# Performance work log

Hardware: AMD Instinct MI355X
Metric: run time of the kernel (lower is better)

Reference implementation:

```python
import jax, jax.numpy as jnp
import numpy as np

B, T, N, F = 32, 24, 1024, 2   # batch, seq_len, num_adj, num_feature
HID = 32                       # opt['hidden_dim']
U = HID // 2                   # rnn_units = 16
TF = 31                        # opt['time_feature']


def setup_inputs():
    key = jax.random.key(0)
    ks = jax.random.split(key, 40)
    def nrm(k, shape):
        return jax.random.normal(k, shape, dtype=jnp.float32) * 0.05
    inp = {}
    inp['recent_data'] = nrm(ks[0], (B, T, N, F))
    inp['trend_data'] = nrm(ks[1], (B, T, F))
    # normalized adjacency-like matrix (non-negative, row mass ~1)
    inp['sub_graph'] = jax.random.uniform(ks[2], (B, N, N), dtype=jnp.float32) * (2.0 / N)
    inp['time_feature'] = nrm(ks[3], (B, TF))
    i = 4
    for layer, insz in ((1, F + U), (2, U + U)):
        for g in 'ruc':
            inp[f'gru{layer}_{g}W'] = nrm(ks[i], (U, insz)); i += 1
            inp[f'gru{layer}_{g}b'] = jnp.zeros((U,), jnp.float32)
    for l, insz in ((0, F), (1, HID)):
        inp[f'lstm_Wih{l}'] = nrm(ks[i], (4 * HID, insz)); i += 1
        inp[f'lstm_Whh{l}'] = nrm(ks[i], (4 * HID, HID)); i += 1
        inp[f'lstm_bih{l}'] = jnp.zeros((4 * HID,), jnp.float32)
        inp[f'lstm_bhh{l}'] = jnp.zeros((4 * HID,), jnp.float32)
    inp['ff_W'] = nrm(ks[i], (HID, TF)); i += 1
    inp['ff_b'] = jnp.zeros((HID,), jnp.float32)
    inp['gcn_W'] = nrm(ks[i], (F, int(HID * 2.5))); i += 1
    inp['gcn_b'] = jnp.zeros((F,), jnp.float32)
    return inp


def _gcn(x, A, W, b, act):
    # x: (B,N,in), A: (B,N,N) -> act(fc(A @ x)): (B,N,out)
    return act(jnp.einsum('bij,bjf->bif', A, x) @ W.T + b)


def _gru_cell(x, h, A, rW, rb, uW, ub, cW, cb):
    xh = jnp.concatenate([x, h], axis=-1)
    r = _gcn(xh, A, rW, rb, jax.nn.sigmoid)
    u = _gcn(xh, A, uW, ub, jax.nn.sigmoid)
    c = _gcn(jnp.concatenate([x, r * h], axis=-1), A, cW, cb, jnp.tanh)
    return u * h + (1.0 - u) * c


def _lstm_layer(xs, Wih, Whh, bih, bhh):
    # xs: (T, B, in) -> hidden sequence (T, B, H); PyTorch gate order i,f,g,o
    H = Whh.shape[1]
    z = jnp.zeros((xs.shape[1], H), xs.dtype)
    def step(carry, x_t):
        h, c = carry
        g = x_t @ Wih.T + h @ Whh.T + bih + bhh
        i, f, gg, o = jnp.split(g, 4, axis=-1)
        c = jax.nn.sigmoid(f) * c + jax.nn.sigmoid(i) * jnp.tanh(gg)
        h = jax.nn.sigmoid(o) * jnp.tanh(c)
        return (h, c), h
    _, hs = jax.lax.scan(step, (z, z), xs)
    return hs


def _forward(recent_data, trend_data, sub_graph, time_feature,
             gru1_rW, gru1_rb, gru1_uW, gru1_ub, gru1_cW, gru1_cb,
             gru2_rW, gru2_rb, gru2_uW, gru2_ub, gru2_cW, gru2_cb,
             lstm_Wih0, lstm_Whh0, lstm_bih0, lstm_bhh0,
             lstm_Wih1, lstm_Whh1, lstm_bih1, lstm_bhh1,
             ff_W, ff_b, gcn_W, gcn_b):
    b, t, n, _ = recent_data.shape
    u = gru1_rW.shape[0]
    h0 = jnp.zeros((b, n, u), recent_data.dtype)
    # 2-layer GCGRU encoder over time (only final output/state is used)
    def step(carry, x_t):
        h1, h2 = carry
        h1 = _gru_cell(x_t, h1, sub_graph, gru1_rW, gru1_rb, gru1_uW, gru1_ub, gru1_cW, gru1_cb)
        h2 = _gru_cell(h1, h2, sub_graph, gru2_rW, gru2_rb, gru2_uW, gru2_ub, gru2_cW, gru2_cb)
        return (h1, h2), None
    (h1, h2), _ = jax.lax.scan(step, (h0, h0), jnp.swapaxes(recent_data, 0, 1))
    recent = h2  # (B, N, U)
    # 2-layer LSTM on trend_data; take last timestep hidden
    xs = jnp.swapaxes(trend_data, 0, 1)  # (T, B, F)
    hs = _lstm_layer(xs, lstm_Wih0, lstm_Whh0, lstm_bih0, lstm_bhh0)
    hs = _lstm_layer(hs, lstm_Wih1, lstm_Whh1, lstm_bih1, lstm_bhh1)
    trend = jnp.broadcast_to(hs[-1][:, None, :], (b, n, hs.shape[-1]))
    feat = jax.nn.relu(time_feature @ ff_W.T + ff_b)
    feat = jnp.broadcast_to(feat[:, None, :], (b, n, feat.shape[-1]))
    combined = jnp.concatenate([recent, trend, feat], axis=-1)  # (B, N, 2.5*HID)
    return _gcn(combined, sub_graph, gcn_W, gcn_b, jnp.tanh)  # (B, N, F)


def reference(recent_data, trend_data, sub_graph, time_feature,
              gru1_rW, gru1_rb, gru1_uW, gru1_ub, gru1_cW, gru1_cb,
              gru2_rW, gru2_rb, gru2_uW, gru2_ub, gru2_cW, gru2_cb,
              lstm_Wih0, lstm_Whh0, lstm_bih0, lstm_bhh0,
              lstm_Wih1, lstm_Whh1, lstm_bih1, lstm_bhh1,
              ff_W, ff_b, gcn_W, gcn_b):
    return _forward(recent_data, trend_data, sub_graph, time_feature,
                    gru1_rW, gru1_rb, gru1_uW, gru1_ub, gru1_cW, gru1_cb,
                    gru2_rW, gru2_rb, gru2_uW, gru2_ub, gru2_cW, gru2_cb,
                    lstm_Wih0, lstm_Whh0, lstm_bih0, lstm_bhh0,
                    lstm_Wih1, lstm_Whh1, lstm_bih1, lstm_bhh1,
                    ff_W, ff_b, gcn_W, gcn_b)
```

## Files before the change

kernel.cpp:

```cpp
#include <hip/hip_runtime.h>
#include <cmath>
#include <stdint.h>

#define BB 32
#define TT 24
#define NN 1024
#define FF 2
#define UU 16
#define HH 32
#define TFN 31
#define NWG 256

typedef __attribute__((ext_vector_type(8))) short bf16x8;
typedef __attribute__((ext_vector_type(4))) float f32x4;
typedef unsigned short u16;
typedef unsigned int   u32;
typedef __attribute__((ext_vector_type(4))) u32 u32x4;

__device__ __align__(16) u16 g_Y[2][BB][32*NN];
__device__ float g_c2[BB*FF];
__device__ __align__(256) u32 g_bar[BB][64];
__device__ u32 g_xcdmask[BB];

__device__ __forceinline__ float sigmf(float x){ return 1.f/(1.f+expf(-x)); }
__device__ __forceinline__ u16 f2bf(float f){
  u32 u = __float_as_uint(f);
  return (u16)((u + 0x7fffu + ((u>>16)&1u)) >> 16);
}
__device__ __forceinline__ void ywr(u16* Yb, int j, int n, float s, bool modeA){
  u16* p = (u16*)((char*)Yb + (j<<11) + (((n<<1)) ^ ((j&7)<<4)));
  u16 v = f2bf(s);
  if (modeA) *p = v;
  else __hip_atomic_store(p, v, __ATOMIC_RELAXED, __HIP_MEMORY_SCOPE_AGENT);
}

__device__ __forceinline__ void bbar(u32* cnt, u32 target){
  __syncthreads();
  if (threadIdx.x == 0){
    __hip_atomic_fetch_add(cnt, 1u, __ATOMIC_RELAXED, __HIP_MEMORY_SCOPE_AGENT);
    while (__hip_atomic_load(cnt, __ATOMIC_RELAXED, __HIP_MEMORY_SCOPE_AGENT) < target)
      __builtin_amdgcn_s_sleep(1);
  }
  __syncthreads();
}

template<int W>
__device__ __forceinline__ void stageY(const u16* __restrict__ Yb, u16* Ys,
                                       int tid, bool modeA){
  u32x4 r[W/4];
  if (modeA){
#pragma unroll
    for (int q=0;q<W/4;q++){
      const char* src = (const char*)Yb + q*8192 + tid*16;
      asm volatile("global_load_dwordx4 %0, %1, off sc0"
                   : "=v"(r[q]) : "v"(src));
    }
  } else {
#pragma unroll
    for (int q=0;q<W/4;q++){
      const char* src = (const char*)Yb + q*8192 + tid*16;
      asm volatile("global_load_dwordx4 %0, %1, off sc0 sc1"
                   : "=v"(r[q]) : "v"(src));
    }
  }
  asm volatile("s_waitcnt vmcnt(0)" ::: "memory");
  __builtin_amdgcn_sched_barrier(0);
#pragma unroll
  for (int q=0;q<W/4;q++)
    *(u32x4*)((char*)Ys + q*8192 + tid*16) = r[q];
}

__device__ __forceinline__ void mm32(const bf16x8 (&areg)[32], const u16* Ys,
                                     int base0, int cflip, f32x4& a0, f32x4& a1){
#pragma unroll
  for (int c=0;c<32;c++){
    int off = base0 + ((c ^ cflip) << 6);
    bf16x8 b0 = *(const bf16x8*)((const char*)Ys + off);
    bf16x8 b1 = *(const bf16x8*)((const char*)Ys + off + 32768);
    a0 = __builtin_amdgcn_mfma_f32_16x16x32_bf16(areg[c], b0, a0, 0, 0, 0);
    a1 = __builtin_amdgcn_mfma_f32_16x16x32_bf16(areg[c], b1, a1, 0, 0, 0);
  }
}
__device__ __forceinline__ void mm16(const bf16x8 (&areg)[32], const u16* Ys,
                                     int base0, int cflip, f32x4& a0){
#pragma unroll
  for (int c=0;c<32;c++){
    int off = base0 + ((c ^ cflip) << 6);
    bf16x8 b0 = *(const bf16x8*)((const char*)Ys + off);
    a0 = __builtin_amdgcn_mfma_f32_16x16x32_bf16(areg[c], b0, a0, 0, 0, 0);
  }
}

__global__ __launch_bounds__(128)
void k_lstm(const float* __restrict__ trend, const float* __restrict__ tfeat,
            const float* __restrict__ Wih0, const float* __restrict__ Whh0,
            const float* __restrict__ bih0, const float* __restrict__ bhh0,
            const float* __restrict__ Wih1, const float* __restrict__ Whh1,
            const float* __restrict__ bih1, const float* __restrict__ bhh1,
            const float* __restrict__ ffW, const float* __restrict__ ffb,
            const float* __restrict__ gcnW) {
  __shared__ float h[HH], c[HH], g[4*HH], hs0[TT][HH], tr[HH], fe[HH];
  int b = blockIdx.x, tid = threadIdx.x;
  if (tid == 0){
    __hip_atomic_store(&g_bar[b][0], 0u, __ATOMIC_RELAXED, __HIP_MEMORY_SCOPE_AGENT);
    __hip_atomic_store(&g_xcdmask[b], 0u, __ATOMIC_RELAXED, __HIP_MEMORY_SCOPE_AGENT);
  }
  if (tid < HH) { h[tid]=0.f; c[tid]=0.f; }
  __syncthreads();
  for (int t=0;t<TT;t++) {
    float x0 = trend[(b*TT+t)*FF+0], x1 = trend[(b*TT+t)*FF+1];
    float gv = bih0[tid] + bhh0[tid] + x0*Wih0[tid*FF+0] + x1*Wih0[tid*FF+1];
#pragma unroll
    for (int k=0;k<HH;k++) gv += h[k]*Whh0[tid*HH+k];
    g[tid] = gv;
    __syncthreads();
    if (tid < HH) {
      float ii = sigmf(g[tid]), ff = sigmf(g[HH+tid]);
      float gg = tanhf(g[2*HH+tid]), oo = sigmf(g[3*HH+tid]);
      float cn = ff*c[tid] + ii*gg;
      c[tid] = cn;
      float hn = oo*tanhf(cn);
      h[tid] = hn;
      hs0[t][tid] = hn;
    }
    __syncthreads();
  }
  if (tid < HH) { h[tid]=0.f; c[tid]=0.f; }
  __syncthreads();
  for (int t=0;t<TT;t++) {
    float gv = bih1[tid] + bhh1[tid];
#pragma unroll
    for (int k=0;k<HH;k++) gv += hs0[t][k]*Wih1[tid*HH+k];
#pragma unroll
    for (int k=0;k<HH;k++) gv += h[k]*Whh1[tid*HH+k];
    g[tid] = gv;
    __syncthreads();
    if (tid < HH) {
      float ii = sigmf(g[tid]), ff = sigmf(g[HH+tid]);
      float gg = tanhf(g[2*HH+tid]), oo = sigmf(g[3*HH+tid]);
      float cn = ff*c[tid] + ii*gg;
      c[tid] = cn;
      h[tid] = oo*tanhf(cn);
    }
    __syncthreads();
  }
  if (tid < HH) {
    tr[tid] = h[tid];
    float fv = ffb[tid];
#pragma unroll
    for (int j=0;j<TFN;j++) fv += tfeat[b*TFN+j]*ffW[tid*TFN+j];
    fe[tid] = fmaxf(fv, 0.f);
  }
  __syncthreads();
  if (tid < FF) {
    float s = 0.f;
#pragma unroll
    for (int j=0;j<HH;j++) s += tr[j]*gcnW[tid*80+16+j];
#pragma unroll
    for (int j=0;j<HH;j++) s += fe[j]*gcnW[tid*80+48+j];
    g_c2[b*FF+tid] = s;
  }
}

struct KP {
  const float *recent, *A;
  const float *g1rW,*g1rb,*g1uW,*g1ub,*g1cW,*g1cb;
  const float *g2rW,*g2rb,*g2uW,*g2ub,*g2cW,*g2cb;
  const float *gcnW,*gcnb;
  float *out;
};

__global__ __launch_bounds__(512, 2)
void k_main(KP p){
  __shared__ __align__(16) u16 Ys[32*NN];
  __shared__ float Ps [128][33];
  __shared__ float h1s[128][17];
  __shared__ float h2s[128][17];
  __shared__ float us_[128][17];
  __shared__ float rhs[128][17];

  const int wg = blockIdx.x;
  const int b = (wg & 7)*4 + (wg >> 6);
  const int i0 = ((wg >> 3) & 7) << 7;
  const int tid = threadIdx.x;
  const int v = tid >> 6, lane = tid & 63, m = lane & 15, quad = lane >> 4;
  const int rloc = v << 4;
  const int row = tid >> 2, jj = tid & 3;
  const int n = i0 + row;
  const int base0 = m*2048 + ((quad ^ (m & 3)) << 4);
  const int cflip = (m >> 2) & 1;
  u32* bar = &g_bar[b][0];

  if (tid == 0){
    u32 xcc;
    asm volatile("s_getreg_b32 %0, hwreg(HW_REG_XCC_ID)" : "=s"(xcc));
    __hip_atomic_fetch_or(&g_xcdmask[b], 1u << (xcc & 31),
                          __ATOMIC_RELAXED, __HIP_MEMORY_SCOPE_AGENT);
  }

  bf16x8 areg[32];
  {
    const float* Ab = p.A + ((size_t)(b*NN + i0 + rloc + m))*NN + quad*8;
#pragma unroll
    for (int c=0;c<32;c++){
      float4 f0 = *(const float4*)(Ab + c*32);
      float4 f1 = *(const float4*)(Ab + c*32 + 4);
      bf16x8 tv;
      tv[0]=(short)f2bf(f0.x); tv[1]=(short)f2bf(f0.y);
      tv[2]=(short)f2bf(f0.z); tv[3]=(short)f2bf(f0.w);
      tv[4]=(short)f2bf(f1.x); tv[5]=(short)f2bf(f1.y);
      tv[6]=(short)f2bf(f1.z); tv[7]=(short)f2bf(f1.w);
      areg[c] = tv;
    }
  }

#pragma unroll
  for (int q=0;q<4;q++){ h1s[row][jj*4+q]=0.f; h2s[row][jj*4+q]=0.f; }

  {
    const float* xr = p.recent + (((size_t)b*TT)*NN + n)*FF;
    float x0 = xr[0], x1 = xr[1];
    u16* Yb = g_Y[0][b];
#pragma unroll
    for (int m2=0;m2<8;m2++){
      int j = jj*8 + m2;
      const float* W = (j<16) ? (p.g1rW + j*18) : (p.g1uW + (j-16)*18);
      ywr(Yb, j, n, x0*W[0] + x1*W[1], false);
    }
  }
  u32 gen = 0;
  bbar(bar, (++gen)*8);

  const u32 mk = __hip_atomic_load(&g_xcdmask[b], __ATOMIC_RELAXED,
                                   __HIP_MEMORY_SCOPE_AGENT);
  const bool modeA = (__popc(mk) == 1);

  int buf = 0;
  for (int t=0;t<TT;t++){
    stageY<32>(g_Y[buf][b], Ys, tid, modeA);
    __syncthreads();
    {
      f32x4 a0={0.f,0.f,0.f,0.f}, a1={0.f,0.f,0.f,0.f};
      mm32(areg, Ys, base0, cflip, a0, a1);
#pragma unroll
      for (int r=0;r<4;r++){
        Ps[rloc + quad*4 + r][m]    = a0[r];
        Ps[rloc + quad*4 + r][16+m] = a1[r];
      }
    }
    __syncthreads();
#pragma unroll
    for (int q=0;q<4;q++){
      int j = jj*4+q;
      float rv = sigmf(Ps[row][j]    + p.g1rb[j]);
      float uv = sigmf(Ps[row][16+j] + p.g1ub[j]);
      us_[row][j] = uv;
      rhs[row][j] = rv * h1s[row][j];
    }
    __syncthreads();
    {
      const float* xr = p.recent + (((size_t)b*TT + t)*NN + n)*FF;
      float x0 = xr[0], x1 = xr[1];
      u16* Yb = g_Y[buf^1][b];
#pragma unroll
      for (int q=0;q<4;q++){
        int j = jj*4+q;
        const float* W = p.g1cW + j*18;
        float s = fmaf(x0, W[0], x1*W[1]);
#pragma unroll
        for (int f=0;f<16;f++) s = fmaf(rhs[row][f], W[2+f], s);
        ywr(Yb, j, n, s, modeA);
      }
    }
    bbar(bar, (++gen)*8); buf ^= 1;

    stageY<16>(g_Y[buf][b], Ys, tid, modeA);
    __syncthreads();
    {
      f32x4 a0={0.f,0.f,0.f,0.f};
      mm16(areg, Ys, base0, cflip, a0);
#pragma unroll
      for (int r=0;r<4;r++) Ps[rloc + quad*4 + r][m] = a0[r];
    }
    __syncthreads();
#pragma unroll
    for (int q=0;q<4;q++){
      int j = jj*4+q;
      float cv = tanhf(Ps[row][j] + p.g1cb[j]);
      float uv = us_[row][j];
      h1s[row][j] = uv*h1s[row][j] + (1.f-uv)*cv;
    }
    __syncthreads();
    {
      u16* Yb = g_Y[buf^1][b];
#pragma unroll
      for (int m2=0;m2<8;m2++){
        int j = jj*8 + m2;
        const float* W = (j<16) ? (p.g2rW + j*32) : (p.g2uW + (j-16)*32);
        float s = 0.f;
#pragma unroll
        for (int f=0;f<16;f++) s = fmaf(h1s[row][f], W[f],    s);
#pragma unroll
        for (int f=0;f<16;f++) s = fmaf(h2s[row][f], W[16+f], s);
        ywr(Yb, j, n, s, modeA);
      }
    }
    bbar(bar, (++gen)*8); buf ^= 1;

    stageY<32>(g_Y[buf][b], Ys, tid, modeA);
    __syncthreads();
    {
      f32x4 a0={0.f,0.f,0.f,0.f}, a1={0.f,0.f,0.f,0.f};
      mm32(areg, Ys, base0, cflip, a0, a1);
#pragma unroll
      for (int r=0;r<4;r++){
        Ps[rloc + quad*4 + r][m]    = a0[r];
        Ps[rloc + quad*4 + r][16+m] = a1[r];
      }
    }
    __syncthreads();
#pragma unroll
    for (int q=0;q<4;q++){
      int j = jj*4+q;
      float rv = sigmf(Ps[row][j]    + p.g2rb[j]);
      float uv = sigmf(Ps[row][16+j] + p.g2ub[j]);
      us_[row][j] = uv;
      rhs[row][j] = rv * h2s[row][j];
    }
    __syncthreads();
    {
      u16* Yb = g_Y[buf^1][b];
#pragma unroll
      for (int q=0;q<4;q++){
        int j = jj*4+q;
        const float* W = p.g2cW + j*32;
        float s = 0.f;
#pragma unroll
        for (int f=0;f<16;f++) s = fmaf(h1s[row][f], W[f],    s);
#pragma unroll
        for (int f=0;f<16;f++) s = fmaf(rhs[row][f], W[16+f], s);
        ywr(Yb, j, n, s, modeA);
      }
    }
    bbar(bar, (++gen)*8); buf ^= 1;

    stageY<16>(g_Y[buf][b], Ys, tid, modeA);
    __syncthreads();
    {
      f32x4 a0={0.f,0.f,0.f,0.f};
      mm16(areg, Ys, base0, cflip, a0);
#pragma unroll
      for (int r=0;r<4;r++) Ps[rloc + quad*4 + r][m] = a0[r];
    }
    __syncthreads();
#pragma unroll
    for (int q=0;q<4;q++){
      int j = jj*4+q;
      float cv = tanhf(Ps[row][j] + p.g2cb[j]);
      float uv = us_[row][j];
      h2s[row][j] = uv*h2s[row][j] + (1.f-uv)*cv;
    }
    __syncthreads();
    if (t < TT-1){
      const float* xr = p.recent + (((size_t)b*TT + t + 1)*NN + n)*FF;
      float x0 = xr[0], x1 = xr[1];
      u16* Yb = g_Y[buf^1][b];
#pragma unroll
      for (int m2=0;m2<8;m2++){
        int j = jj*8 + m2;
        const float* W = (j<16) ? (p.g1rW + j*18) : (p.g1uW + (j-16)*18);
        float s = fmaf(x0, W[0], x1*W[1]);
#pragma unroll
        for (int f=0;f<16;f++) s = fmaf(h1s[row][f], W[2+f], s);
        ywr(Yb, j, n, s, modeA);
      }
    } else {
      u16* Yb = g_Y[buf^1][b];
#pragma unroll
      for (int q=0;q<4;q++){
        int j = jj*4+q;
        float s = 0.f;
        if (j < FF){
          s = g_c2[b*FF + j];
#pragma unroll
          for (int f=0;f<16;f++) s = fmaf(h2s[row][f], p.gcnW[j*80+f], s);
        }
        ywr(Yb, j, n, s, modeA);
      }
    }
    bbar(bar, (++gen)*8); buf ^= 1;
  }

  stageY<16>(g_Y[buf][b], Ys, tid, modeA);
  __syncthreads();
  {
    f32x4 a0={0.f,0.f,0.f,0.f};
    mm16(areg, Ys, base0, cflip, a0);
    if (m < FF){
      float bb = p.gcnb[m];
#pragma unroll
      for (int r=0;r<4;r++){
        int nn = i0 + rloc + quad*4 + r;
        p.out[((size_t)b*NN + nn)*FF + m] = tanhf(a0[r] + bb);
      }
    }
  }
}

extern "C" void kernel_launch(void* const* d_in, const int* in_sizes, int n_in,
                              void* d_out, int out_size, void* d_ws, size_t ws_size,
                              hipStream_t stream) {
  (void)in_sizes; (void)n_in; (void)d_ws; (void)ws_size; (void)out_size;
  const float* recent = (const float*)d_in[0];
  const float* trend  = (const float*)d_in[1];
  const float* A      = (const float*)d_in[2];
  const float* tfeat  = (const float*)d_in[3];
  const float* g1rW = (const float*)d_in[4];  const float* g1rb = (const float*)d_in[5];
  const float* g1uW = (const float*)d_in[6];  const float* g1ub = (const float*)d_in[7];
  const float* g1cW = (const float*)d_in[8];  const float* g1cb = (const float*)d_in[9];
  const float* g2rW = (const float*)d_in[10]; const float* g2rb = (const float*)d_in[11];
  const float* g2uW = (const float*)d_in[12]; const float* g2ub = (const float*)d_in[13];
  const float* g2cW = (const float*)d_in[14]; const float* g2cb = (const float*)d_in[15];
  const float* Wih0 = (const float*)d_in[16]; const float* Whh0 = (const float*)d_in[17];
  const float* bih0 = (const float*)d_in[18]; const float* bhh0 = (const float*)d_in[19];
  const float* Wih1 = (const float*)d_in[20]; const float* Whh1 = (const float*)d_in[21];
  const float* bih1 = (const float*)d_in[22]; const float* bhh1 = (const float*)d_in[23];
  const float* ffW  = (const float*)d_in[24]; const float* ffb  = (const float*)d_in[25];
  const float* gcnW = (const float*)d_in[26]; const float* gcnb = (const float*)d_in[27];
  float* out = (float*)d_out;

  k_lstm<<<BB, 128, 0, stream>>>(trend, tfeat, Wih0, Whh0, bih0, bhh0,
                                 Wih1, Whh1, bih1, bhh1, ffW, ffb, gcnW);

  KP kp;
  kp.recent = recent; kp.A = A;
  kp.g1rW=g1rW; kp.g1rb=g1rb; kp.g1uW=g1uW; kp.g1ub=g1ub; kp.g1cW=g1cW; kp.g1cb=g1cb;
  kp.g2rW=g2rW; kp.g2rb=g2rb; kp.g2uW=g2uW; kp.g2ub=g2ub; kp.g2cW=g2cW; kp.g2cb=g2cb;
  kp.gcnW=gcnW; kp.gcnb=gcnb; kp.out=out;
  void* args[] = { (void*)&kp };
  hipLaunchCooperativeKernel((const void*)k_main, dim3(NWG), dim3(512), args, 0, stream);
}
```

Baseline: 1.605 ms.

## Hoist next-step layer-1 GRU input into layer-2 phase to drop a grid barrier

Replaces the two ping-pong Y buffers with dedicated per-stage regions (two alternating RU1 slots, C1, RU2, C2). This lets the next timestep's layer-1 r/u projections be written during the layer-2 r/u phase, removing one cross-workgroup barrier per timestep (4 instead of 5). The barrier spin also gets an iteration cap and a longer sleep after a few polls. The cap risks proceeding early under contention, and the longer sleep can add wake-up latency.

After: 1.638 ms. 1.02x slower.

```diff
diff --git a/kernel.cpp b/kernel.cpp
--- a/kernel.cpp
+++ b/kernel.cpp
@@ -17,7 +17,12 @@
 typedef unsigned int   u32;
 typedef __attribute__((ext_vector_type(4))) u32 u32x4;
 
-__device__ __align__(16) u16 g_Y[2][BB][32*NN];
+#define RU1A 0
+#define RU1B 32
+#define C1R  64
+#define RU2R 80
+#define C2R  112
+__device__ __align__(16) u16 g_Y[BB][128*NN];
 __device__ float g_c2[BB*FF];
 __device__ __align__(256) u32 g_bar[BB][64];
 __device__ u32 g_xcdmask[BB];
@@ -37,9 +42,15 @@
 __device__ __forceinline__ void bbar(u32* cnt, u32 target){
   __syncthreads();
   if (threadIdx.x == 0){
-    __hip_atomic_fetch_add(cnt, 1u, __ATOMIC_RELAXED, __HIP_MEMORY_SCOPE_AGENT);
-    while (__hip_atomic_load(cnt, __ATOMIC_RELAXED, __HIP_MEMORY_SCOPE_AGENT) < target)
-      __builtin_amdgcn_s_sleep(1);
+    u32 old = __hip_atomic_fetch_add(cnt, 1u, __ATOMIC_RELAXED, __HIP_MEMORY_SCOPE_AGENT);
+    if (old + 1u < target){
+      for (u32 it=0; it<200000u; ++it){
+        if (__hip_atomic_load(cnt, __ATOMIC_RELAXED, __HIP_MEMORY_SCOPE_AGENT) >= target)
+          break;
+        if (it < 4) __builtin_amdgcn_s_sleep(1);
+        else        __builtin_amdgcn_s_sleep(4);
+      }
+    }
   }
   __syncthreads();
 }
@@ -102,7 +113,7 @@
   __shared__ float h[HH], c[HH], g[4*HH], hs0[TT][HH], tr[HH], fe[HH];
   int b = blockIdx.x, tid = threadIdx.x;
   if (tid == 0){
-    __hip_atomic_store(&g_bar[b][0], 0u, __ATOMIC_RELAXED, __HIP_MEMORY_SCOPE_AGENT);
+    __hip_atomic_store(&g_bar[b][0],  0u, __ATOMIC_RELAXED, __HIP_MEMORY_SCOPE_AGENT);
     __hip_atomic_store(&g_xcdmask[b], 0u, __ATOMIC_RELAXED, __HIP_MEMORY_SCOPE_AGENT);
   }
   if (tid < HH) { h[tid]=0.f; c[tid]=0.f; }
@@ -190,12 +201,14 @@
   const int base0 = m*2048 + ((quad ^ (m & 3)) << 4);
   const int cflip = (m >> 2) & 1;
   u32* bar = &g_bar[b][0];
+  u16* Yb  = &g_Y[b][0];
 
   if (tid == 0){
     u32 xcc;
     asm volatile("s_getreg_b32 %0, hwreg(HW_REG_XCC_ID)" : "=s"(xcc));
-    __hip_atomic_fetch_or(&g_xcdmask[b], 1u << (xcc & 31),
-                          __ATOMIC_RELAXED, __HIP_MEMORY_SCOPE_AGENT);
+    u32 oldm = __hip_atomic_fetch_or(&g_xcdmask[b], 1u << (xcc & 31),
+                                     __ATOMIC_RELAXED, __HIP_MEMORY_SCOPE_AGENT);
+    asm volatile("" :: "v"(oldm));
   }
 
   bf16x8 areg[32];
@@ -220,12 +233,12 @@
   {
     const float* xr = p.recent + (((size_t)b*TT)*NN + n)*FF;
     float x0 = xr[0], x1 = xr[1];
-    u16* Yb = g_Y[0][b];
+    u16* Yr = Yb + RU1A*NN;
 #pragma unroll
     for (int m2=0;m2<8;m2++){
       int j = jj*8 + m2;
       const float* W = (j<16) ? (p.g1rW + j*18) : (p.g1uW + (j-16)*18);
-      ywr(Yb, j, n, x0*W[0] + x1*W[1], false);
+      ywr(Yr, j, n, x0*W[0] + x1*W[1], false);
     }
   }
   u32 gen = 0;
@@ -235,9 +248,8 @@
                                    __HIP_MEMORY_SCOPE_AGENT);
   const bool modeA = (__popc(mk) == 1);
 
-  int buf = 0;
   for (int t=0;t<TT;t++){
-    stageY<32>(g_Y[buf][b], Ys, tid, modeA);
+    stageY<32>(Yb + ((t&1) ? RU1B : RU1A)*NN, Ys, tid, modeA);
     __syncthreads();
     {
       f32x4 a0={0.f,0.f,0.f,0.f}, a1={0.f,0.f,0.f,0.f};
@@ -261,7 +273,7 @@
     {
       const float* xr = p.recent + (((size_t)b*TT + t)*NN + n)*FF;
       float x0 = xr[0], x1 = xr[1];
-      u16* Yb = g_Y[buf^1][b];
+      u16* Yc = Yb + C1R*NN;
 #pragma unroll
       for (int q=0;q<4;q++){
         int j = jj*4+q;
@@ -269,12 +281,12 @@
         float s = fmaf(x0, W[0], x1*W[1]);
 #pragma unroll
         for (int f=0;f<16;f++) s = fmaf(rhs[row][f], W[2+f], s);
-        ywr(Yb, j, n, s, modeA);
-      }
-    }
-    bbar(bar, (++gen)*8); buf ^= 1;
-
-    stageY<16>(g_Y[buf][b], Ys, tid, modeA);
+        ywr(Yc, j, n, s, modeA);
+      }
+    }
+    bbar(bar, (++gen)*8);
+
+    stageY<16>(Yb + C1R*NN, Ys, tid, modeA);
     __syncthreads();
     {
       f32x4 a0={0.f,0.f,0.f,0.f};
@@ -292,7 +304,7 @@
     }
     __syncthreads();
     {
-      u16* Yb = g_Y[buf^1][b];
+      u16* Yr2 = Yb + RU2R*NN;
 #pragma unroll
       for (int m2=0;m2<8;m2++){
         int j = jj*8 + m2;
@@ -302,12 +314,26 @@
         for (int f=0;f<16;f++) s = fmaf(h1s[row][f], W[f],    s);
 #pragma unroll
         for (int f=0;f<16;f++) s = fmaf(h2s[row][f], W[16+f], s);
-        ywr(Yb, j, n, s, modeA);
-      }
-    }
-    bbar(bar, (++gen)*8); buf ^= 1;
-
-    stageY<32>(g_Y[buf][b], Ys, tid, modeA);
+        ywr(Yr2, j, n, s, modeA);
+      }
+      if (t < TT-1){
+        const float* xr = p.recent + (((size_t)b*TT + t + 1)*NN + n)*FF;
+        float x0 = xr[0], x1 = xr[1];
+        u16* Yr1 = Yb + (((t+1)&1) ? RU1B : RU1A)*NN;
+#pragma unroll
+        for (int m2=0;m2<8;m2++){
+          int j = jj*8 + m2;
+          const float* W = (j<16) ? (p.g1rW + j*18) : (p.g1uW + (j-16)*18);
+          float s = fmaf(x0, W[0], x1*W[1]);
+#pragma unroll
+          for (int f=0;f<16;f++) s = fmaf(h1s[row][f], W[2+f], s);
+          ywr(Yr1, j, n, s, modeA);
+        }
+      }
+    }
+    bbar(bar, (++gen)*8);
+
+    stageY<32>(Yb + RU2R*NN, Ys, tid, modeA);
     __syncthreads();
     {
       f32x4 a0={0.f,0.f,0.f,0.f}, a1={0.f,0.f,0.f,0.f};
@@ -329,7 +355,7 @@
     }
     __syncthreads();
     {
-      u16* Yb = g_Y[buf^1][b];
+      u16* Yc2 = Yb + C2R*NN;
 #pragma unroll
       for (int q=0;q<4;q++){
         int j = jj*4+q;
@@ -339,12 +365,12 @@
         for (int f=0;f<16;f++) s = fmaf(h1s[row][f], W[f],    s);
 #pragma unroll
         for (int f=0;f<16;f++) s = fmaf(rhs[row][f], W[16+f], s);
-        ywr(Yb, j, n, s, modeA);
-      }
-    }
-    bbar(bar, (++gen)*8); buf ^= 1;
-
-    stageY<16>(g_Y[buf][b], Ys, tid, modeA);
+        ywr(Yc2, j, n, s, modeA);
+      }
+    }
+    bbar(bar, (++gen)*8);
+
+    stageY<16>(Yb + C2R*NN, Ys, tid, modeA);
     __syncthreads();
     {
       f32x4 a0={0.f,0.f,0.f,0.f};
@@ -361,21 +387,8 @@
       h2s[row][j] = uv*h2s[row][j] + (1.f-uv)*cv;
     }
     __syncthreads();
-    if (t < TT-1){
-      const float* xr = p.recent + (((size_t)b*TT + t + 1)*NN + n)*FF;
-      float x0 = xr[0], x1 = xr[1];
-      u16* Yb = g_Y[buf^1][b];
-#pragma unroll
-      for (int m2=0;m2<8;m2++){
-        int j = jj*8 + m2;
-        const float* W = (j<16) ? (p.g1rW + j*18) : (p.g1uW + (j-16)*18);
-        float s = fmaf(x0, W[0], x1*W[1]);
-#pragma unroll
-        for (int f=0;f<16;f++) s = fmaf(h1s[row][f], W[2+f], s);
-        ywr(Yb, j, n, s, modeA);
-      }
-    } else {
-      u16* Yb = g_Y[buf^1][b];
+    if (t == TT-1){
+      u16* Yc = Yb + C1R*NN;
 #pragma unroll
       for (int q=0;q<4;q++){
         int j = jj*4+q;
@@ -385,13 +398,13 @@
 #pragma unroll
           for (int f=0;f<16;f++) s = fmaf(h2s[row][f], p.gcnW[j*80+f], s);
         }
-        ywr(Yb, j, n, s, modeA);
-      }
-    }
-    bbar(bar, (++gen)*8); buf ^= 1;
-  }
-
-  stageY<16>(g_Y[buf][b], Ys, tid, modeA);
+        ywr(Yc, j, n, s, modeA);
+      }
+      bbar(bar, (++gen)*8);
+    }
+  }
+
+  stageY<16>(Yb + C1R*NN, Ys, tid, modeA);
   __syncthreads();
   {
     f32x4 a0={0.f,0.f,0.f,0.f};
```
